# Optimization experiments

Measured on AMD Instinct MI355X. Metric: run time of the kernel, lower is better.

## Reference

```python
import jax, jax.numpy as jnp
import numpy as np

K = 8           # neighbor_num
H = 8           # n_heads
DH = 64         # dim_single_head


def setup_inputs() -> dict:
    key = jax.random.key(0)
    ks = jax.random.split(key, 6)
    B, N, D = 2, 8192, 256
    inner = H * DH  # 512
    x = jax.random.normal(ks[0], (B, N, D), jnp.float32)
    center_pos3d = jax.random.normal(ks[1], (B, N, 3), jnp.float32)
    Wq = jax.random.normal(ks[2], (D, inner), jnp.float32) * 0.02
    Wkv = jax.random.normal(ks[3], (D, 2 * inner), jnp.float32) * 0.02
    Wout = jax.random.normal(ks[4], (inner, D), jnp.float32) * 0.02
    bout = jnp.zeros((D,), jnp.float32)
    return {"x": x, "center_pos3d": center_pos3d, "Wq": Wq, "Wkv": Wkv,
            "Wout": Wout, "bout": bout}


def _knn_idx(pos, k):
    # pos: [B,N,3] -> indices of k nearest neighbors per point, [B,N,k]
    sq = jnp.sum(pos * pos, axis=-1)                      # [B,N]
    d2 = sq[:, :, None] + sq[:, None, :] - 2.0 * jnp.einsum('bnc,bmc->bnm', pos, pos)
    _, idx = jax.lax.top_k(-d2, k)                        # smallest distances
    return idx


def reference(x, center_pos3d, Wq, Wkv, Wout, bout):
    B, N, D = x.shape
    inner = H * DH
    scale = DH ** -0.5

    idx = _knn_idx(center_pos3d, K)                       # [B,N,K] int32
    # grouping_operation: gather neighbor features -> [B,N,K,D]
    knn_x = jax.vmap(lambda xb, ib: xb[ib])(x, idx)

    q = (x @ Wq).reshape(B, N, H, DH)                     # [B,N,H,DH]
    kv = knn_x @ Wkv                                      # [B,N,K,2*inner]
    k_, v_ = jnp.split(kv, 2, axis=-1)
    k_ = k_.reshape(B, N, K, H, DH)
    v_ = v_.reshape(B, N, K, H, DH)

    dots = jnp.einsum('bnhd,bnkhd->bnhk', q, k_) * scale  # [B,N,H,K]
    attn = jax.nn.softmax(dots, axis=-1)
    out = jnp.einsum('bnhk,bnkhd->bnhd', attn, v_)        # [B,N,H,DH]
    out = out.reshape(B, N, inner)
    return out @ Wout + bout                              # dropout p=0 -> identity
```

## Files before the change

### kernel.cpp

```cpp
#include <hip/hip_runtime.h>
#include <hip/hip_bf16.h>

#define N_PTS 8192
#define KNN 8

typedef __attribute__((ext_vector_type(8))) short short8;
typedef __attribute__((ext_vector_type(4))) float float4v;
typedef unsigned long long u64;

static __device__ __forceinline__ short f2bf(float f) {
    unsigned u = __float_as_uint(f);
    unsigned r = (u + 0x7FFFu + ((u >> 16) & 1u)) >> 16;
    return (short)r;
}
static __device__ __forceinline__ float bf2f(short s) {
    return __uint_as_float(((unsigned)(unsigned short)s) << 16);
}

static __device__ __forceinline__ unsigned sortkey(float f) {
    unsigned u = __float_as_uint(f);
    return u ^ (((unsigned)((int)u >> 31)) | 0x80000000u);
}

static __device__ __forceinline__ void ins8(u64* best, u64 x) {
#pragma unroll
    for (int j = 0; j < 8; ++j) {
        const u64 lo = x < best[j] ? x : best[j];
        const u64 hi = x < best[j] ? best[j] : x;
        best[j] = lo; x = hi;
    }
}

__global__ __launch_bounds__(256) void fused_knn_conv(const float* __restrict__ pos,
                                                      u64* __restrict__ partial,
                                                      const float* __restrict__ x,
                                                      const float* __restrict__ Wq,
                                                      const float* __restrict__ Wkv,
                                                      const float* __restrict__ Wout,
                                                      short* __restrict__ xb,
                                                      short* __restrict__ wqkvt,
                                                      short* __restrict__ woutt)
{
    __shared__ __align__(16) char smem[16896];
    const int tid = threadIdx.x;
    const int g5 = blockIdx.x / 5;
    const int r5 = blockIdx.x % 5;

    if (r5 == 0) {
        const int kb = g5;
        float4* cand = (float4*)smem;
        unsigned short* buf = (unsigned short*)(smem + 8192);

        const int p   = kb & 15;
        const int qg  = kb >> 4;
        const int batch = qg >> 5;
        const int q_in_b = (qg & 31) * 256 + tid;
        const float* bpos = pos + (long)batch * N_PTS * 3;

        if (tid < 128) {
            const float* src = bpos + (p * 512 + tid * 4) * 3;
            const float4 f0 = *(const float4*)(src);
            const float4 f1 = *(const float4*)(src + 4);
            const float4 f2 = *(const float4*)(src + 8);
            const int c0 = tid * 4;
            cand[c0 + 0] = make_float4(f0.x, f0.y, f0.z,
                                       fmaf(f0.x, f0.x, fmaf(f0.y, f0.y, f0.z * f0.z)));
            cand[c0 + 1] = make_float4(f0.w, f1.x, f1.y,
                                       fmaf(f0.w, f0.w, fmaf(f1.x, f1.x, f1.y * f1.y)));
            cand[c0 + 2] = make_float4(f1.z, f1.w, f2.x,
                                       fmaf(f1.z, f1.z, fmaf(f1.w, f1.w, f2.x * f2.x)));
            cand[c0 + 3] = make_float4(f2.y, f2.z, f2.w,
                                       fmaf(f2.y, f2.y, fmaf(f2.z, f2.z, f2.w * f2.w)));
        }
        __syncthreads();

        const float qx = bpos[q_in_b * 3 + 0];
        const float qy = bpos[q_in_b * 3 + 1];
        const float qz = bpos[q_in_b * 3 + 2];
        const float nqx = -2.0f * qx;
        const float nqy = -2.0f * qy;
        const float nqz = -2.0f * qz;

        float bmin[32];
#pragma unroll
        for (int j = 0; j < 32; ++j) bmin[j] = 3.0e38f;

        for (int base = 0; base < 512; base += 32) {
#pragma unroll
            for (int g = 0; g < 32; ++g) {
                const float4 c = cand[base + g];
                bmin[g] = fminf(bmin[g],
                                fmaf(c.x, nqx, fmaf(c.y, nqy, fmaf(c.z, nqz, c.w))));
            }
        }

        float t8[8];
#pragma unroll
        for (int j = 0; j < 8; ++j) t8[j] = 3.0e38f;
#pragma unroll
        for (int i = 0; i < 32; ++i) {
            float x_ = bmin[i];
#pragma unroll
            for (int j = 0; j < 8; ++j) {
                const float lo = fminf(t8[j], x_);
                const float hi = fmaxf(t8[j], x_);
                t8[j] = lo; x_ = hi;
            }
        }
        const float t = t8[7];

        int cnt = 0;
        for (int base = 0; base < 512; base += 32) {
#pragma unroll
            for (int g = 0; g < 32; ++g) {
                const float4 c = cand[base + g];
                const float d = fmaf(c.x, nqx, fmaf(c.y, nqy, fmaf(c.z, nqz, c.w)));
                if (d <= t) {
                    buf[tid * 17 + (cnt < 16 ? cnt : 16)] = (unsigned short)(base + g);
                    ++cnt;
                }
            }
        }

        u64 best[8];
#pragma unroll
        for (int j = 0; j < 8; ++j) best[j] = ~0ULL;

        if (cnt <= 16) {
            for (int u = 0; u < cnt; ++u) {
                const int i = buf[tid * 17 + u];
                const float4 c = cand[i];
                const float d = fmaf(c.x, nqx, fmaf(c.y, nqy, fmaf(c.z, nqz, c.w)));
                ins8(best, ((u64)sortkey(d) << 32) | (unsigned)(p * 512 + i));
            }
        } else {
            for (int i = 0; i < 512; ++i) {
                const float4 c = cand[i];
                const float d = fmaf(c.x, nqx, fmaf(c.y, nqy, fmaf(c.z, nqz, c.w)));
                const u64 x_ = ((u64)sortkey(d) << 32) | (unsigned)(p * 512 + i);
                if (x_ < best[7]) ins8(best, x_);
            }
        }

        const long qglob = (long)batch * N_PTS + q_in_b;
#pragma unroll
        for (int j = 0; j < 8; ++j)
            partial[(long)(p * 8 + j) * 16384 + qglob] = best[j];

    } else {
        const int bid = g5 * 4 + (r5 - 1);
        if (bid < 2048) {
            const int i = bid * 256 + tid;
            const float4 a = ((const float4*)x)[i * 2];
            const float4 b = ((const float4*)x)[i * 2 + 1];
            short8 w = {f2bf(a.x), f2bf(a.y), f2bf(a.z), f2bf(a.w),
                        f2bf(b.x), f2bf(b.y), f2bf(b.z), f2bf(b.w)};
            ((short8*)xb)[i] = w;
        } else if (bid < 2560) {
            const int o = (bid - 2048) * 256 + tid;
            const int n = o >> 8, k = o & 255;
            wqkvt[o] = f2bf(Wq[(long)k * 512 + n]);
        } else if (bid < 3584) {
            const int o = (bid - 2560) * 256 + tid;
            const int n = o >> 8, k = o & 255;
            wqkvt[131072 + o] = f2bf(Wkv[(long)k * 1024 + n]);
        } else {
            const int o = (bid - 3584) * 256 + tid;
            const int n = o >> 9, k = o & 511;
            woutt[o] = f2bf(Wout[(long)k * 256 + n]);
        }
    }
}

__global__ __launch_bounds__(256) void fused_gemm_merge(const short* __restrict__ A,
                                                        const short* __restrict__ Bt,
                                                        short* __restrict__ qall,
                                                        short* __restrict__ kvall,
                                                        const u64* __restrict__ partial,
                                                        int* __restrict__ idxo)
{
    __shared__ short As[128][40];
    __shared__ short Bs[128][40];

    const int tid = threadIdx.x;

    if (blockIdx.x < 64) {
        const int q = blockIdx.x * 256 + tid;
        u64 best[8];
#pragma unroll
        for (int j = 0; j < 8; ++j) best[j] = ~0ULL;
        for (int s = 0; s < 128; ++s) {
            u64 x = partial[(long)s * 16384 + q];
            if (x < best[7]) ins8(best, x);
        }
#pragma unroll
        for (int j = 0; j < 8; ++j)
            idxo[(long)q * 8 + j] = (int)(best[j] & 0xFFFFFFFFu);
        return;
    }

    const int id = blockIdx.x - 64;
    const int bx = id % 12;
    const int by = id / 12;

    const int lane = tid & 63;
    const int wv   = tid >> 6;
    const int quad = lane >> 4;
    const int l15  = lane & 15;
    const int m0 = by * 128;
    const int n0 = bx * 128;
    const int mh = (wv & 1) * 64, nh = (wv >> 1) * 64;

    const int srow  = tid >> 1;
    const int shalf = (tid & 1) * 16;
    const int Kd = 256;

    float4v acc[4][4];
#pragma unroll
    for (int i = 0; i < 4; ++i)
#pragma unroll
        for (int j = 0; j < 4; ++j) acc[i][j] = (float4v)(0.f);

    for (int k0 = 0; k0 < Kd; k0 += 32) {
        const short8* asrc = (const short8*)(A + (long)(m0 + srow) * Kd + k0 + shalf);
        const short8* bsrc = (const short8*)(Bt + (long)(n0 + srow) * Kd + k0 + shalf);
        *(short8*)&As[srow][shalf]     = asrc[0];
        *(short8*)&As[srow][shalf + 8] = asrc[1];
        *(short8*)&Bs[srow][shalf]     = bsrc[0];
        *(short8*)&Bs[srow][shalf + 8] = bsrc[1];
        __syncthreads();

        short8 af[4], bfv[4];
#pragma unroll
        for (int i = 0; i < 4; ++i)
            af[i] = *(const short8*)&As[mh + i * 16 + l15][quad * 8];
#pragma unroll
        for (int j = 0; j < 4; ++j)
            bfv[j] = *(const short8*)&Bs[nh + j * 16 + l15][quad * 8];
#pragma unroll
        for (int i = 0; i < 4; ++i)
#pragma unroll
            for (int j = 0; j < 4; ++j)
                acc[i][j] = __builtin_amdgcn_mfma_f32_16x16x32_bf16(af[i], bfv[j], acc[i][j], 0, 0, 0);
        __syncthreads();
    }

    short* Cb;
    int stride, cb;
    if (n0 < 512) { Cb = qall;  stride = 512;  cb = n0; }
    else          { Cb = kvall; stride = 1024; cb = n0 - 512; }

#pragma unroll
    for (int i = 0; i < 4; ++i)
#pragma unroll
        for (int j = 0; j < 4; ++j) {
            const int col = cb + nh + j * 16 + l15;
#pragma unroll
            for (int r = 0; r < 4; ++r) {
                const int row = m0 + mh + i * 16 + quad * 4 + r;
                Cb[(long)row * stride + col] = f2bf(acc[i][j][r]);
            }
        }
}

__global__ __launch_bounds__(256) void attn_kernel(const short* qall,
                                                   const short* __restrict__ kvall,
                                                   const int* __restrict__ idxp,
                                                   short* outp)
{
    __shared__ float attn_s[4][8][8];
    const int wave = threadIdx.x >> 6;
    const int lane = threadIdx.x & 63;
    const int g = blockIdx.x * 4 + wave;
    const int b = g >> 13;
    const int* myidx = idxp + (long)g * 8;

    {
        const int h = lane >> 3;
        const int k = lane & 7;
        const int j = myidx[k];
        const short8* qrow = (const short8*)(qall + (long)g * 512 + h * 64);
        const short8* krow = (const short8*)(kvall + ((long)(b * N_PTS + j)) * 1024 + h * 64);

        float dot = 0.f;
#pragma unroll
        for (int c = 0; c < 8; ++c) {
            const short8 qv = qrow[c];
            const short8 kv = krow[c];
#pragma unroll
            for (int e = 0; e < 8; ++e)
                dot = fmaf(bf2f(qv[e]), bf2f(kv[e]), dot);
        }
        dot *= 0.125f;

        float m = dot;
#pragma unroll
        for (int off = 1; off < 8; off <<= 1)
            m = fmaxf(m, __shfl_xor(m, off, 8));
        const float e = __expf(dot - m);
        float ssum = e;
#pragma unroll
        for (int off = 1; off < 8; off <<= 1)
            ssum += __shfl_xor(ssum, off, 8);
        attn_s[wave][h][k] = e / ssum;
    }
    __syncthreads();

    const int d8 = lane * 8;
    const int h2 = lane >> 3;
    float o[8] = {0.f, 0.f, 0.f, 0.f, 0.f, 0.f, 0.f, 0.f};
#pragma unroll
    for (int kk = 0; kk < 8; ++kk) {
        const int jj = myidx[kk];
        const float w = attn_s[wave][h2][kk];
        const short8 v = *(const short8*)(kvall + ((long)(b * N_PTS + jj)) * 1024 + 512 + d8);
#pragma unroll
        for (int e = 0; e < 8; ++e)
            o[e] = fmaf(w, bf2f(v[e]), o[e]);
    }
    short8 ov = {f2bf(o[0]), f2bf(o[1]), f2bf(o[2]), f2bf(o[3]),
                 f2bf(o[4]), f2bf(o[5]), f2bf(o[6]), f2bf(o[7])};
    *(short8*)(outp + (long)g * 512 + d8) = ov;
}

__global__ __launch_bounds__(256) void gemm_out(const short* __restrict__ A,
                                                const short* __restrict__ Bt,
                                                const float* __restrict__ bias,
                                                float* __restrict__ C,
                                                int N, int Kd)
{
    __shared__ short As[128][40];
    __shared__ short Bs[128][40];

    const int tid  = threadIdx.x;
    const int lane = tid & 63;
    const int wv   = tid >> 6;
    const int quad = lane >> 4;
    const int l15  = lane & 15;
    const int m0 = blockIdx.y * 128;
    const int n0 = blockIdx.x * 128;
    const int mh = (wv & 1) * 64, nh = (wv >> 1) * 64;

    const int srow  = tid >> 1;
    const int shalf = (tid & 1) * 16;

    float4v acc[4][4];
#pragma unroll
    for (int i = 0; i < 4; ++i)
#pragma unroll
        for (int j = 0; j < 4; ++j) acc[i][j] = (float4v)(0.f);

    for (int k0 = 0; k0 < Kd; k0 += 32) {
        const short8* asrc = (const short8*)(A + (long)(m0 + srow) * Kd + k0 + shalf);
        const short8* bsrc = (const short8*)(Bt + (long)(n0 + srow) * Kd + k0 + shalf);
        *(short8*)&As[srow][shalf]     = asrc[0];
        *(short8*)&As[srow][shalf + 8] = asrc[1];
        *(short8*)&Bs[srow][shalf]     = bsrc[0];
        *(short8*)&Bs[srow][shalf + 8] = bsrc[1];
        __syncthreads();

        short8 af[4], bfv[4];
#pragma unroll
        for (int i = 0; i < 4; ++i)
            af[i] = *(const short8*)&As[mh + i * 16 + l15][quad * 8];
#pragma unroll
        for (int j = 0; j < 4; ++j)
            bfv[j] = *(const short8*)&Bs[nh + j * 16 + l15][quad * 8];
#pragma unroll
        for (int i = 0; i < 4; ++i)
#pragma unroll
            for (int j = 0; j < 4; ++j)
                acc[i][j] = __builtin_amdgcn_mfma_f32_16x16x32_bf16(af[i], bfv[j], acc[i][j], 0, 0, 0);
        __syncthreads();
    }

#pragma unroll
    for (int i = 0; i < 4; ++i)
#pragma unroll
        for (int j = 0; j < 4; ++j) {
            const int col = n0 + nh + j * 16 + l15;
            const float bb = bias[col];
#pragma unroll
            for (int r = 0; r < 4; ++r) {
                const int row = m0 + mh + i * 16 + quad * 4 + r;
                C[(long)row * N + col] = acc[i][j][r] + bb;
            }
        }
}

extern "C" void kernel_launch(void* const* d_in, const int* in_sizes, int n_in,
                              void* d_out, int out_size, void* d_ws, size_t ws_size,
                              hipStream_t stream)
{
    const float* x    = (const float*)d_in[0];
    const float* pos  = (const float*)d_in[1];
    const float* Wq   = (const float*)d_in[2];
    const float* Wkv  = (const float*)d_in[3];
    const float* Wout = (const float*)d_in[4];
    const float* bout = (const float*)d_in[5];
    float* out = (float*)d_out;

    const int M = 16384;

    char* ws = (char*)d_ws;
    int*   idxp  = (int*)ws;                          ws += 1 << 19;
    short* qall  = (short*)ws;                        ws += (long)M * 512 * 2;
    short* kvall = (short*)ws;                        ws += (long)M * 1024 * 2;
    short* xb    = (short*)ws;                        ws += (long)M * 256 * 2;
    short* wqkvt = (short*)ws;                        ws += 1536 * 256 * 2;
    short* woutt = (short*)ws;                        ws += 256 * 512 * 2;
    u64*  partial = (u64*)ws;                         ws += (long)128 * 16384 * 8;

    fused_knn_conv<<<5120, 256, 0, stream>>>(pos, partial, x, Wq, Wkv, Wout,
                                             xb, wqkvt, woutt);
    fused_gemm_merge<<<1600, 256, 0, stream>>>(xb, wqkvt, qall, kvall, partial, idxp);
    attn_kernel<<<M / 4, 256, 0, stream>>>(qall, kvall, idxp, qall);
    gemm_out<<<dim3(2, 128), 256, 0, stream>>>(qall, woutt, bout, out, 256, 512);
}
```

Measured before the change: 303.4 us.

## Split kNN into 32 candidate partitions reading prepacked positions from global memory

Adds a pack_pos kernel that precomputes xyz plus squared norm as float4, and the kNN blocks now read candidates directly from global/L1 instead of staging them in LDS. Candidate partitions go from 16 to 32 of 256 points each, doubling kNN block count and raising occupancy via launch_bounds(256,8). Candidate collection becomes branchless. The extra partial results are stored in the output buffer as scratch, which doubles the merge work in fused_gemm_merge and adds one more launch.

```diff
diff --git a/kernel.cpp b/kernel.cpp
--- a/kernel.cpp
+++ b/kernel.cpp
@@ -31,64 +31,54 @@
     }
 }
 
-__global__ __launch_bounds__(256) void fused_knn_conv(const float* __restrict__ pos,
-                                                      u64* __restrict__ partial,
-                                                      const float* __restrict__ x,
-                                                      const float* __restrict__ Wq,
-                                                      const float* __restrict__ Wkv,
-                                                      const float* __restrict__ Wout,
-                                                      short* __restrict__ xb,
-                                                      short* __restrict__ wqkvt,
-                                                      short* __restrict__ woutt)
-{
-    __shared__ __align__(16) char smem[16896];
+__global__ __launch_bounds__(256) void pack_pos(const float* __restrict__ pos,
+                                                float4* __restrict__ packed)
+{
+    const int i = blockIdx.x * 256 + threadIdx.x;
+    const float x = pos[i * 3 + 0];
+    const float y = pos[i * 3 + 1];
+    const float z = pos[i * 3 + 2];
+    packed[i] = make_float4(x, y, z, fmaf(x, x, fmaf(y, y, z * z)));
+}
+
+__global__ __launch_bounds__(256, 8) void fused_knn_conv(const float4* __restrict__ packed,
+                                                         u64* __restrict__ partial,
+                                                         u64* __restrict__ partial2,
+                                                         const float* __restrict__ x,
+                                                         const float* __restrict__ Wq,
+                                                         const float* __restrict__ Wkv,
+                                                         const float* __restrict__ Wout,
+                                                         short* __restrict__ xb,
+                                                         short* __restrict__ wqkvt,
+                                                         short* __restrict__ woutt)
+{
+    __shared__ unsigned short buf[256 * 17];
     const int tid = threadIdx.x;
-    const int g5 = blockIdx.x / 5;
-    const int r5 = blockIdx.x % 5;
-
-    if (r5 == 0) {
-        const int kb = g5;
-        float4* cand = (float4*)smem;
-        unsigned short* buf = (unsigned short*)(smem + 8192);
-
-        const int p   = kb & 15;
-        const int qg  = kb >> 4;
+    const int g3 = blockIdx.x / 3;
+    const int r3 = blockIdx.x % 3;
+
+    if (r3 == 0) {
+        const int kb = g3;
+        const int p  = kb & 31;
+        const int qg = kb >> 5;
         const int batch = qg >> 5;
         const int q_in_b = (qg & 31) * 256 + tid;
-        const float* bpos = pos + (long)batch * N_PTS * 3;
-
-        if (tid < 128) {
-            const float* src = bpos + (p * 512 + tid * 4) * 3;
-            const float4 f0 = *(const float4*)(src);
-            const float4 f1 = *(const float4*)(src + 4);
-            const float4 f2 = *(const float4*)(src + 8);
-            const int c0 = tid * 4;
-            cand[c0 + 0] = make_float4(f0.x, f0.y, f0.z,
-                                       fmaf(f0.x, f0.x, fmaf(f0.y, f0.y, f0.z * f0.z)));
-            cand[c0 + 1] = make_float4(f0.w, f1.x, f1.y,
-                                       fmaf(f0.w, f0.w, fmaf(f1.x, f1.x, f1.y * f1.y)));
-            cand[c0 + 2] = make_float4(f1.z, f1.w, f2.x,
-                                       fmaf(f1.z, f1.z, fmaf(f1.w, f1.w, f2.x * f2.x)));
-            cand[c0 + 3] = make_float4(f2.y, f2.z, f2.w,
-                                       fmaf(f2.y, f2.y, fmaf(f2.z, f2.z, f2.w * f2.w)));
-        }
-        __syncthreads();
-
-        const float qx = bpos[q_in_b * 3 + 0];
-        const float qy = bpos[q_in_b * 3 + 1];
-        const float qz = bpos[q_in_b * 3 + 2];
-        const float nqx = -2.0f * qx;
-        const float nqy = -2.0f * qy;
-        const float nqz = -2.0f * qz;
+
+        const float4* __restrict__ cands = packed + batch * N_PTS + p * 256;
+
+        const float4 q4 = packed[batch * N_PTS + q_in_b];
+        const float nqx = -2.0f * q4.x;
+        const float nqy = -2.0f * q4.y;
+        const float nqz = -2.0f * q4.z;
 
         float bmin[32];
 #pragma unroll
         for (int j = 0; j < 32; ++j) bmin[j] = 3.0e38f;
 
-        for (int base = 0; base < 512; base += 32) {
+        for (int base = 0; base < 256; base += 32) {
 #pragma unroll
             for (int g = 0; g < 32; ++g) {
-                const float4 c = cand[base + g];
+                const float4 c = cands[base + g];
                 bmin[g] = fminf(bmin[g],
                                 fmaf(c.x, nqx, fmaf(c.y, nqy, fmaf(c.z, nqz, c.w))));
             }
@@ -109,16 +99,15 @@
         }
         const float t = t8[7];
 
+        const int bbase = tid * 17;
         int cnt = 0;
-        for (int base = 0; base < 512; base += 32) {
+        for (int base = 0; base < 256; base += 32) {
 #pragma unroll
             for (int g = 0; g < 32; ++g) {
-                const float4 c = cand[base + g];
+                const float4 c = cands[base + g];
                 const float d = fmaf(c.x, nqx, fmaf(c.y, nqy, fmaf(c.z, nqz, c.w)));
-                if (d <= t) {
-                    buf[tid * 17 + (cnt < 16 ? cnt : 16)] = (unsigned short)(base + g);
-                    ++cnt;
-                }
+                buf[bbase + (cnt < 16 ? cnt : 16)] = (unsigned short)(base + g);
+                cnt += (d <= t) ? 1 : 0;
             }
         }
 
@@ -128,27 +117,29 @@
 
         if (cnt <= 16) {
             for (int u = 0; u < cnt; ++u) {
-                const int i = buf[tid * 17 + u];
-                const float4 c = cand[i];
+                const int i = buf[bbase + u];
+                const float4 c = cands[i];
                 const float d = fmaf(c.x, nqx, fmaf(c.y, nqy, fmaf(c.z, nqz, c.w)));
-                ins8(best, ((u64)sortkey(d) << 32) | (unsigned)(p * 512 + i));
+                ins8(best, ((u64)sortkey(d) << 32) | (unsigned)(p * 256 + i));
             }
         } else {
-            for (int i = 0; i < 512; ++i) {
-                const float4 c = cand[i];
+            for (int i = 0; i < 256; ++i) {
+                const float4 c = cands[i];
                 const float d = fmaf(c.x, nqx, fmaf(c.y, nqy, fmaf(c.z, nqz, c.w)));
-                const u64 x_ = ((u64)sortkey(d) << 32) | (unsigned)(p * 512 + i);
+                const u64 x_ = ((u64)sortkey(d) << 32) | (unsigned)(p * 256 + i);
                 if (x_ < best[7]) ins8(best, x_);
             }
         }
 
         const long qglob = (long)batch * N_PTS + q_in_b;
+        u64* __restrict__ pb = (p < 16 ? partial : partial2)
+                             + (long)((p & 15) * 8) * 16384;
 #pragma unroll
         for (int j = 0; j < 8; ++j)
-            partial[(long)(p * 8 + j) * 16384 + qglob] = best[j];
+            pb[(long)j * 16384 + qglob] = best[j];
 
     } else {
-        const int bid = g5 * 4 + (r5 - 1);
+        const int bid = g3 * 2 + (r3 - 1);
         if (bid < 2048) {
             const int i = bid * 256 + tid;
             const float4 a = ((const float4*)x)[i * 2];
@@ -177,6 +168,7 @@
                                                         short* __restrict__ qall,
                                                         short* __restrict__ kvall,
                                                         const u64* __restrict__ partial,
+                                                        const u64* __restrict__ partial2,
                                                         int* __restrict__ idxo)
 {
     __shared__ short As[128][40];
@@ -191,6 +183,10 @@
         for (int j = 0; j < 8; ++j) best[j] = ~0ULL;
         for (int s = 0; s < 128; ++s) {
             u64 x = partial[(long)s * 16384 + q];
+            if (x < best[7]) ins8(best, x);
+        }
+        for (int s = 0; s < 128; ++s) {
+            u64 x = partial2[(long)s * 16384 + q];
             if (x < best[7]) ins8(best, x);
         }
 #pragma unroll
@@ -410,10 +406,14 @@
     short* wqkvt = (short*)ws;                        ws += 1536 * 256 * 2;
     short* woutt = (short*)ws;                        ws += 256 * 512 * 2;
     u64*  partial = (u64*)ws;                         ws += (long)128 * 16384 * 8;
-
-    fused_knn_conv<<<5120, 256, 0, stream>>>(pos, partial, x, Wq, Wkv, Wout,
-                                             xb, wqkvt, woutt);
-    fused_gemm_merge<<<1600, 256, 0, stream>>>(xb, wqkvt, qall, kvall, partial, idxp);
+    float4* packed = (float4*)ws;                     ws += (long)M * 16;
+    u64* partial2 = (u64*)d_out;
+
+    pack_pos<<<64, 256, 0, stream>>>(pos, packed);
+    fused_knn_conv<<<6144, 256, 0, stream>>>(packed, partial, partial2, x,
+                                             Wq, Wkv, Wout, xb, wqkvt, woutt);
+    fused_gemm_merge<<<1600, 256, 0, stream>>>(xb, wqkvt, qall, kvall,
+                                               partial, partial2, idxp);
     attn_kernel<<<M / 4, 256, 0, stream>>>(qall, kvall, idxp, qall);
     gemm_out<<<dim3(2, 128), 256, 0, stream>>>(qall, woutt, bout, out, 256, 512);
 }
```

After: 343.6 us. +13.2%, slower.
